# Optimization experiments

Hardware: AMD Instinct MI355X
Metric: run time of the kernel (lower is better)

The kernel has to match this reference:

```python
import jax, jax.numpy as jnp
import numpy as np

N, E, B = 8192, 131072, 256
F_ATOM, D, H, HD, L, FC, BINS = 92, 256, 8, 32, 6, 512, 256
VMIN, VMAX = 0.0, 8.0


def layer_norm(x, g, b, eps=1e-5):
    mu = jnp.mean(x, axis=-1, keepdims=True)
    var = jnp.var(x, axis=-1, keepdims=True)
    return (x - mu) * jax.lax.rsqrt(var + eps) * g + b


def silu(x):
    return x * jax.nn.sigmoid(x)


def setup_inputs() -> dict:
    key = jax.random.key(0)
    ks = iter(jax.random.split(key, 80))

    def lin(fan_in, shape):
        return jax.random.normal(next(ks), shape, jnp.float32) / np.sqrt(fan_in)

    inp = {
        'x': jax.random.normal(next(ks), (N, F_ATOM), jnp.float32),
        'edge_attr': jax.random.normal(next(ks), (E, 3), jnp.float32) * 2.0,
        'edge_index': jax.random.randint(next(ks), (2, E), 0, N, dtype=jnp.int32),
        'batch': jnp.sort(jax.random.randint(next(ks), (N,), 0, B, dtype=jnp.int32)),
        # atom_embedding: Linear(92,256) -> LN -> SiLU -> Linear(256,256)
        'aw1': lin(F_ATOM, (F_ATOM, D)), 'ab1': jnp.zeros((D,)),
        'ag1': jnp.ones((D,)), 'abt1': jnp.zeros((D,)),
        'aw2': lin(D, (D, D)), 'ab2': jnp.zeros((D,)),
        # rbf MLP: Linear(256,256) LN SiLU Linear LN SiLU Linear
        'rw1': lin(BINS, (BINS, D)), 'rb1': jnp.zeros((D,)),
        'rg1': jnp.ones((D,)), 'rbt1': jnp.zeros((D,)),
        'rw2': lin(D, (D, D)), 'rb2': jnp.zeros((D,)),
        'rg2': jnp.ones((D,)), 'rbt2': jnp.zeros((D,)),
        'rw3': lin(D, (D, D)), 'rb3': jnp.zeros((D,)),
        # L stacked PrdnetConv (edge-conditioned multi-head graph attention)
        'Wq': lin(D, (L, D, D)), 'bq': jnp.zeros((L, D)),
        'Wk': lin(D, (L, D, D)), 'bk': jnp.zeros((L, D)),
        'Wv': lin(D, (L, D, D)), 'bv': jnp.zeros((L, D)),
        'We': lin(D, (L, D, D)), 'be': jnp.zeros((L, D)),
        'Wo': lin(D, (L, D, D)), 'bo': jnp.zeros((L, D)),
        'lng': jnp.ones((L, D)), 'lnb': jnp.zeros((L, D)),
        # FC head: Linear(256,512) then fc_out Linear(512,1)
        'fw1': lin(D, (D, FC)), 'fb1': jnp.zeros((FC,)),
        'fow': lin(FC, (FC, 1)), 'fob': jnp.zeros((1,)),
    }
    return inp


def _forward(x, edge_attr, edge_index, batch, aw1, ab1, ag1, abt1, aw2, ab2,
             rw1, rb1, rg1, rbt1, rw2, rb2, rg2, rbt2, rw3, rb3,
             Wq, bq, Wk, bk, Wv, bv, We, be, Wo, bo, lng, lnb,
             fw1, fb1, fow, fob):
    # atom embedding (dropout = identity at inference)
    node = silu(layer_norm(x @ aw1 + ab1, ag1, abt1)) @ aw2 + ab2  # [N, D]

    # RBF expansion of edge lengths, then edge MLP
    d = jnp.linalg.norm(edge_attr, axis=1)  # [E]
    centers = jnp.linspace(VMIN, VMAX, BINS)
    gamma = 1.0 / (centers[1] - centers[0]) ** 2
    rbf = jnp.exp(-gamma * (d[:, None] - centers[None, :]) ** 2)  # [E, BINS]
    e = silu(layer_norm(rbf @ rw1 + rb1, rg1, rbt1))
    e = silu(layer_norm(e @ rw2 + rb2, rg2, rbt2))
    e = e @ rw3 + rb3  # [E, D]

    src, dst = edge_index[0], edge_index[1]
    inv_sqrt = 1.0 / np.sqrt(HD)
    for l in range(L):
        res = node
        q = (node @ Wq[l] + bq[l]).reshape(N, H, HD)
        k = (node @ Wk[l] + bk[l]).reshape(N, H, HD)
        v = (node @ Wv[l] + bv[l]).reshape(N, H, HD)
        ee = (e @ We[l] + be[l]).reshape(E, H, HD)
        kj = k[src] + ee  # edge-conditioned keys [E, H, HD]
        vj = v[src] + ee  # edge-conditioned values
        score = jnp.sum(q[dst] * kj, axis=-1) * inv_sqrt  # [E, H]
        smax = jax.ops.segment_max(score, dst, num_segments=N)  # [N, H]
        ex = jnp.exp(score - smax[dst])
        den = jax.ops.segment_sum(ex, dst, num_segments=N)
        alpha = ex / (den[dst] + 1e-16)  # neighborhood softmax [E, H]
        msg = jax.ops.segment_sum(alpha[:, :, None] * vj, dst, num_segments=N)
        out = msg.reshape(N, D) @ Wo[l] + bo[l]
        out = layer_norm(out, lng[l], lnb[l])
        node = out + res  # residual

    # scatter-mean graph pooling
    sums = jax.ops.segment_sum(node, batch, num_segments=B)  # [B, D]
    cnt = jax.ops.segment_sum(jnp.ones((N,), node.dtype), batch, num_segments=B)
    feats = sums / jnp.clip(cnt, 1.0)[:, None]

    feats = feats @ fw1 + fb1  # single fc layer: no act (i == len-1 in source)
    return feats @ fow + fob  # [B, 1], identity link


def reference(x, edge_attr, edge_index, batch, aw1, ab1, ag1, abt1, aw2, ab2,
              rw1, rb1, rg1, rbt1, rw2, rb2, rg2, rbt2, rw3, rb3,
              Wq, bq, Wk, bk, Wv, bv, We, be, Wo, bo, lng, lnb,
              fw1, fb1, fow, fob):
    return _forward(x, edge_attr, edge_index, batch, aw1, ab1, ag1, abt1, aw2,
                    ab2, rw1, rb1, rg1, rbt1, rw2, rb2, rg2, rbt2, rw3, rb3,
                    Wq, bq, Wk, bk, Wv, bv, We, be, Wo, bo, lng, lnb,
                    fw1, fb1, fow, fob)
```

## Files before the change

kernel.cpp:

```cpp
#include <hip/hip_runtime.h>
#include <hip/hip_bf16.h>
#include <cstddef>

#define NN    8192
#define EE    131072
#define BB    256
#define F_AT  92
#define DD    256
#define HH    8
#define HDIM  32
#define LL    6
#define FCD   512

typedef __hip_bfloat16 bf16;
typedef __attribute__((ext_vector_type(8))) __bf16 bf16x8;
typedef __attribute__((ext_vector_type(4))) float f32x4;

__device__ __forceinline__ float to_f(float x) { return x; }
__device__ __forceinline__ float to_f(bf16 x) { return __bfloat162float(x); }
__device__ __forceinline__ float bfu(unsigned short u) {
    return __uint_as_float(((unsigned)u) << 16);
}
__device__ __forceinline__ unsigned short bfbits(float x) {
    bf16 h = __float2bfloat16(x);
    return *(unsigned short*)&h;
}
__device__ __forceinline__ void store_v(float* p, float v) { *p = v; }
__device__ __forceinline__ void store_v(bf16* p, float v) { *p = __float2bfloat16(v); }

__device__ __forceinline__ float4 load4(const float* p) { return *(const float4*)p; }
__device__ __forceinline__ float4 load4(const bf16* p) {
    const ushort4 r = *(const ushort4*)p;
    return make_float4(bfu(r.x), bfu(r.y), bfu(r.z), bfu(r.w));
}

__device__ __forceinline__ void store_f4(float* p, const float4& f) {
    *(float4*)p = f;
}
__device__ __forceinline__ void store_f4(bf16* p, const float4& f) {
    ushort4 u = {bfbits(f.x), bfbits(f.y), bfbits(f.z), bfbits(f.w)};
    *(ushort4*)p = u;
}

__device__ __forceinline__ bf16x8 ld8(const bf16* p) { return *(const bf16x8*)p; }
__device__ __forceinline__ bf16x8 ld8(const float* p) {
    const float4 f0 = *(const float4*)p;
    const float4 f1 = *(const float4*)(p + 4);
    bf16x8 r;
    r[0] = (__bf16)f0.x; r[1] = (__bf16)f0.y; r[2] = (__bf16)f0.z; r[3] = (__bf16)f0.w;
    r[4] = (__bf16)f1.x; r[5] = (__bf16)f1.y; r[6] = (__bf16)f1.z; r[7] = (__bf16)f1.w;
    return r;
}

__device__ __forceinline__ void async_copy16(const void* g, void* l) {
    __builtin_amdgcn_global_load_lds(
        (const __attribute__((address_space(1))) unsigned int*)g,
        (__attribute__((address_space(3))) unsigned int*)l, 16, 0, 0);
}

__global__ __launch_bounds__(256) void transpose_weights(
    const float* __restrict__ rw1, const float* __restrict__ rw2,
    const float* __restrict__ rw3, const float* __restrict__ aw2,
    const float* __restrict__ Wq, const float* __restrict__ Wk,
    const float* __restrict__ Wv, const float* __restrict__ We,
    const float* __restrict__ Wo, __bf16* __restrict__ out)
{
    __shared__ float tile[64][65];
    const int midx = blockIdx.y;
    const float* src;
    if (midx == 0) src = rw1;
    else if (midx == 1) src = rw2;
    else if (midx == 2) src = rw3;
    else if (midx == 3) src = aw2;
    else {
        const int l = (midx - 4) / 5, s = (midx - 4) % 5;
        const float* bases[5] = {Wq, Wk, Wv, We, Wo};
        src = bases[s] + (size_t)l * 65536;
    }
    __bf16* dst = out + (size_t)midx * 65536;
    const int k0 = (blockIdx.x >> 2) * 64;
    const int n0 = (blockIdx.x & 3) * 64;
    const int c = threadIdx.x & 63;
    const int r0 = threadIdx.x >> 6;
#pragma unroll
    for (int p = 0; p < 16; ++p) {
        const int r = r0 + p * 4;
        tile[r][c] = src[(size_t)(k0 + r) * 256 + n0 + c];
    }
    __syncthreads();
#pragma unroll
    for (int p = 0; p < 16; ++p) {
        const int n = r0 + p * 4;
        dst[(size_t)(n0 + n) * 256 + k0 + c] = (__bf16)tile[c][n];
    }
}

__global__ __launch_bounds__(256) void pack_qkv_bias(
    const float* __restrict__ bq, const float* __restrict__ bk,
    const float* __restrict__ bv, float* __restrict__ out)
{
    const int i = blockIdx.x * 256 + threadIdx.x;
    if (i >= LL * 768) return;
    const int l = i / 768, r = i % 768;
    const float* s = (r < 256) ? bq : (r < 512) ? bk : bv;
    out[i] = s[l * 256 + (r & 255)];
}

__global__ __launch_bounds__(256) void combine_w3e(
    const float* __restrict__ rw3, const float* __restrict__ We,
    __bf16* __restrict__ Wt_out)
{
    __shared__ float As[16][65];
    __shared__ float Ws[16][65];
    const int l = blockIdx.z;
    const float* W = We + (size_t)l * 65536;
    __bf16* dst = Wt_out + (size_t)l * 65536;
    const int m0 = blockIdx.x * 64;
    const int n0 = blockIdx.y * 64;
    const int tid = threadIdx.x;
    const int tx = tid & 15, ty = tid >> 4;
    float acc[4][4] = {};

    for (int k0 = 0; k0 < 256; k0 += 16) {
        {
            const int ar = tid >> 2;
            const int ac = (tid & 3) * 4;
#pragma unroll
            for (int j = 0; j < 4; ++j)
                As[ac + j][ar] = rw3[(size_t)(m0 + ar) * 256 + k0 + ac + j];
        }
        {
            const int wr = tid >> 4;
            const int wc = (tid & 15) * 4;
#pragma unroll
            for (int j = 0; j < 4; ++j)
                Ws[wr][wc + j] = W[(size_t)(k0 + wr) * 256 + n0 + wc + j];
        }
        __syncthreads();
#pragma unroll
        for (int kk = 0; kk < 16; ++kk) {
            float a[4], b[4];
#pragma unroll
            for (int i = 0; i < 4; ++i) a[i] = As[kk][ty * 4 + i];
#pragma unroll
            for (int j = 0; j < 4; ++j) b[j] = Ws[kk][tx * 4 + j];
#pragma unroll
            for (int i = 0; i < 4; ++i)
#pragma unroll
                for (int j = 0; j < 4; ++j) acc[i][j] += a[i] * b[j];
        }
        __syncthreads();
    }
#pragma unroll
    for (int i = 0; i < 4; ++i) {
        const int gk = m0 + ty * 4 + i;
#pragma unroll
        for (int j = 0; j < 4; ++j) {
            const int gn = n0 + tx * 4 + j;
            dst[(size_t)gn * 256 + gk] = (__bf16)acc[i][j];
        }
    }
}

__global__ __launch_bounds__(256) void combine_bias(
    const float* __restrict__ rb3, const float* __restrict__ We,
    const float* __restrict__ be, float* __restrict__ out)
{
    const int l = blockIdx.x;
    const int n = threadIdx.x;
    const float* W = We + (size_t)l * 65536;
    float s = be[l * 256 + n];
    for (int m = 0; m < 256; ++m) s += rb3[m] * W[m * 256 + n];
    out[l * 256 + n] = s;
}

__global__ __launch_bounds__(256) void mfma_gemm_ln(
    const bf16* __restrict__ A, const __bf16* __restrict__ Wt,
    const float* __restrict__ bias, const float* __restrict__ g,
    const float* __restrict__ b, bf16* __restrict__ C, int do_silu)
{
    __shared__ __align__(16) __bf16 As[64 * 64];
    __shared__ __align__(16) __bf16 Bs[256 * 64];
    const int tid = threadIdx.x;
    const int m0 = blockIdx.x * 64;
    const int wave = tid >> 6, lane = tid & 63;
    const int lm = lane & 15, lq = lane >> 4;
    const int lrow = lane >> 3;
    const int lcolsw = ((lane & 7) ^ lrow) * 8;

    f32x4 acc[16] = {};

    for (int k0 = 0; k0 < 256; k0 += 64) {
#pragma unroll
        for (int p = 0; p < 2; ++p) {
            const int rbase = wave * 16 + p * 8;
            async_copy16(A + (size_t)(m0 + rbase + lrow) * 256 + k0 + lcolsw,
                         As + rbase * 64);
        }
#pragma unroll
        for (int p = 0; p < 8; ++p) {
            const int rbase = wave * 64 + p * 8;
            async_copy16(Wt + (size_t)(rbase + lrow) * 256 + k0 + lcolsw,
                         Bs + rbase * 64);
        }
        __syncthreads();
#pragma unroll
        for (int ks = 0; ks < 2; ++ks) {
            const int sw = ((ks * 4 + lq) ^ (lm & 7)) * 8;
            const bf16x8 a = *(const bf16x8*)(As + (wave * 16 + lm) * 64 + sw);
#pragma unroll
            for (int j = 0; j < 16; ++j) {
                const bf16x8 bf = *(const bf16x8*)(Bs + (j * 16 + lm) * 64 + sw);
                acc[j] = __builtin_amdgcn_mfma_f32_16x16x32_bf16(a, bf, acc[j], 0, 0, 0);
            }
        }
        __syncthreads();
    }

    float gg[16], bb[16];
#pragma unroll
    for (int j = 0; j < 16; ++j) {
        const float bv = bias[j * 16 + lm];
        gg[j] = g[j * 16 + lm];
        bb[j] = b[j * 16 + lm];
#pragma unroll
        for (int r = 0; r < 4; ++r) acc[j][r] += bv;
    }

#pragma unroll
    for (int r = 0; r < 4; ++r) {
        float s = 0.f, q = 0.f;
#pragma unroll
        for (int j = 0; j < 16; ++j) { const float v = acc[j][r]; s += v; q += v * v; }
#pragma unroll
        for (int msk = 1; msk < 16; msk <<= 1) {
            s += __shfl_xor(s, msk);
            q += __shfl_xor(q, msk);
        }
        const float mean = s * (1.f / 256.f);
        const float var = q * (1.f / 256.f) - mean * mean;
        const float rs = rsqrtf(var + 1e-5f);
        bf16* crow = C + (size_t)(m0 + wave * 16 + lq * 4 + r) * 256;
#pragma unroll
        for (int j = 0; j < 16; ++j) {
            float v = (acc[j][r] - mean) * rs * gg[j] + bb[j];
            if (do_silu) v = v / (1.f + __expf(-v));
            crow[j * 16 + lm] = __float2bfloat16(v);
        }
    }
}

template <typename CT>
__global__ __launch_bounds__(256) void mfma_gemm_async(
    const bf16* __restrict__ A, const __bf16* __restrict__ Wt,
    const float* __restrict__ bias, CT* __restrict__ C,
    int M, int Nn, int K)
{
    __shared__ __align__(16) __bf16 As[128 * 64];
    __shared__ __align__(16) __bf16 Bs[128 * 64];
    const int tid = threadIdx.x;
    const int m0 = blockIdx.y * 128;
    const int n0 = blockIdx.x * 128;
    const int wave = tid >> 6, lane = tid & 63;
    const int wm = (wave & 1) * 64, wn = (wave >> 1) * 64;
    const int lm = lane & 15, lq = lane >> 4;
    const int lrow = lane >> 3;
    const int lcolsw = ((lane & 7) ^ lrow) * 8;

    f32x4 acc[4][4] = {};

    for (int k0 = 0; k0 < K; k0 += 64) {
#pragma unroll
        for (int p = 0; p < 4; ++p) {
            const int rbase = wave * 32 + p * 8;
            async_copy16(A  + (size_t)(m0 + rbase + lrow) * K + k0 + lcolsw,
                         As + rbase * 64);
            async_copy16(Wt + (size_t)(n0 + rbase + lrow) * K + k0 + lcolsw,
                         Bs + rbase * 64);
        }
        __syncthreads();
#pragma unroll
        for (int ks = 0; ks < 2; ++ks) {
            const int sw = ((ks * 4 + lq) ^ (lm & 7)) * 8;
            bf16x8 a[4], b[4];
#pragma unroll
            for (int i = 0; i < 4; ++i) {
                a[i] = *(const bf16x8*)(As + (wm + i * 16 + lm) * 64 + sw);
                b[i] = *(const bf16x8*)(Bs + (wn + i * 16 + lm) * 64 + sw);
            }
#pragma unroll
            for (int i = 0; i < 4; ++i)
#pragma unroll
                for (int j = 0; j < 4; ++j)
                    acc[i][j] = __builtin_amdgcn_mfma_f32_16x16x32_bf16(
                        a[i], b[j], acc[i][j], 0, 0, 0);
        }
        __syncthreads();
    }

#pragma unroll
    for (int i = 0; i < 4; ++i) {
        const int gm = m0 + wm + i * 16 + lq * 4;
#pragma unroll
        for (int j = 0; j < 4; ++j) {
            const int gn = n0 + wn + j * 16 + lm;
            const float bv = bias ? bias[gn] : 0.f;
#pragma unroll
            for (int r = 0; r < 4; ++r)
                store_v(&C[(size_t)(gm + r) * Nn + gn], acc[i][j][r] + bv);
        }
    }
}

template <typename AT, typename CT>
__global__ __launch_bounds__(256) void mfma_gemm(
    const AT* __restrict__ A, const __bf16* __restrict__ Wt,
    const float* __restrict__ bias, CT* __restrict__ C,
    int M, int Nn, int K)
{
    __shared__ __align__(16) __bf16 As[128 * 72];
    __shared__ __align__(16) __bf16 Bs[128 * 72];
    const int tid = threadIdx.x;
    const int m0 = blockIdx.x * 128;
    const int n0 = blockIdx.y * 128;
    const int wave = tid >> 6, lane = tid & 63;
    const int wm = (wave & 1) * 64, wn = (wave >> 1) * 64;
    const int lm = lane & 15, lq = lane >> 4;

    f32x4 acc[4][4] = {};

    const int srow = tid >> 3;
    const int scol = (tid & 7) * 8;

    for (int k0 = 0; k0 < K; k0 += 64) {
#pragma unroll
        for (int p = 0; p < 4; ++p) {
            const int r = srow + 32 * p;
            *(bf16x8*)(As + r * 72 + scol) = ld8(A + (size_t)(m0 + r) * K + k0 + scol);
            *(bf16x8*)(Bs + r * 72 + scol) = *(const bf16x8*)(Wt + (size_t)(n0 + r) * K + k0 + scol);
        }
        __syncthreads();
#pragma unroll
        for (int ks = 0; ks < 2; ++ks) {
            bf16x8 a[4], b[4];
#pragma unroll
            for (int i = 0; i < 4; ++i) {
                a[i] = *(const bf16x8*)(As + (wm + i * 16 + lm) * 72 + ks * 32 + lq * 8);
                b[i] = *(const bf16x8*)(Bs + (wn + i * 16 + lm) * 72 + ks * 32 + lq * 8);
            }
#pragma unroll
            for (int i = 0; i < 4; ++i)
#pragma unroll
                for (int j = 0; j < 4; ++j)
                    acc[i][j] = __builtin_amdgcn_mfma_f32_16x16x32_bf16(
                        a[i], b[j], acc[i][j], 0, 0, 0);
        }
        __syncthreads();
    }

#pragma unroll
    for (int i = 0; i < 4; ++i) {
        const int gm = m0 + wm + i * 16 + lq * 4;
#pragma unroll
        for (int j = 0; j < 4; ++j) {
            const int gn = n0 + wn + j * 16 + lm;
            const float bv = bias ? bias[gn] : 0.f;
#pragma unroll
            for (int r = 0; r < 4; ++r)
                store_v(&C[(size_t)(gm + r) * Nn + gn], acc[i][j][r] + bv);
        }
    }
}

template <typename AT, typename CT>
__global__ __launch_bounds__(256) void gemm_bias(
    const AT* __restrict__ A, const float* __restrict__ W,
    const float* __restrict__ bias, CT* __restrict__ C,
    int M, int Nn, int K)
{
    __shared__ float As[16][65];
    __shared__ float Ws[16][65];
    const int m0 = blockIdx.x * 64;
    const int n0 = blockIdx.y * 64;
    const int tid = threadIdx.x;
    const int tx = tid & 15, ty = tid >> 4;
    float acc[4][4] = {};

    for (int k0 = 0; k0 < K; k0 += 16) {
        {
            const int ar = tid >> 2;
            const int ac = (tid & 3) * 4;
            const int gm = m0 + ar;
#pragma unroll
            for (int j = 0; j < 4; ++j) {
                const int gk = k0 + ac + j;
                float v = 0.f;
                if (gm < M && gk < K) v = to_f(A[(size_t)gm * K + gk]);
                As[ac + j][ar] = v;
            }
        }
        {
            const int wr = tid >> 4;
            const int wc = (tid & 15) * 4;
            const int gk = k0 + wr;
#pragma unroll
            for (int j = 0; j < 4; ++j) {
                float v = 0.f;
                if (gk < K) v = W[(size_t)gk * Nn + n0 + wc + j];
                Ws[wr][wc + j] = v;
            }
        }
        __syncthreads();
#pragma unroll
        for (int kk = 0; kk < 16; ++kk) {
            float a[4], b[4];
#pragma unroll
            for (int i = 0; i < 4; ++i) a[i] = As[kk][ty * 4 + i];
#pragma unroll
            for (int j = 0; j < 4; ++j) b[j] = Ws[kk][tx * 4 + j];
#pragma unroll
            for (int i = 0; i < 4; ++i)
#pragma unroll
                for (int j = 0; j < 4; ++j) acc[i][j] += a[i] * b[j];
        }
        __syncthreads();
    }
#pragma unroll
    for (int i = 0; i < 4; ++i) {
        const int gm = m0 + ty * 4 + i;
        if (gm >= M) continue;
#pragma unroll
        for (int j = 0; j < 4; ++j) {
            const int gn = n0 + tx * 4 + j;
            float v = acc[i][j];
            if (bias) v += bias[gn];
            store_v(&C[(size_t)gm * Nn + gn], v);
        }
    }
}

__global__ __launch_bounds__(256) void rbf_kernel(
    const float* __restrict__ ea, const int* __restrict__ eid,
    bf16* __restrict__ rbf)
{
    const int p = blockIdx.x * 4 + (threadIdx.x >> 6);
    const int e = eid[p];
    const int c0 = (threadIdx.x & 63) * 4;
    const float ax = ea[e * 3 + 0];
    const float ay = ea[e * 3 + 1];
    const float az = ea[e * 3 + 2];
    const float d = sqrtf(ax * ax + ay * ay + az * az);
    const float step = 8.0f / 255.0f;
    const float gamma = 1.0f / (step * step);
    float o[4];
#pragma unroll
    for (int j = 0; j < 4; ++j) {
        const float t = d - (float)(c0 + j) * step;
        o[j] = __expf(-gamma * t * t);
    }
    store_f4(rbf + (size_t)p * DD + c0, make_float4(o[0], o[1], o[2], o[3]));
}

template <typename XT, typename YT>
__global__ __launch_bounds__(256) void ln_act_kernel(
    const XT* __restrict__ X, YT* __restrict__ Y,
    const float* __restrict__ g, const float* __restrict__ b,
    const float* __restrict__ resid, int rows, int do_silu)
{
    const int wave = threadIdx.x >> 6;
    const int lane = threadIdx.x & 63;
    const int r = blockIdx.x * 4 + wave;
    if (r >= rows) return;
    const float4 x = load4(X + (size_t)r * DD + lane * 4);
    float s = x.x + x.y + x.z + x.w;
    float q = x.x * x.x + x.y * x.y + x.z * x.z + x.w * x.w;
    for (int off = 32; off; off >>= 1) {
        s += __shfl_down(s, off);
        q += __shfl_down(q, off);
    }
    s = __shfl(s, 0);
    q = __shfl(q, 0);
    const float mean = s * (1.f / 256.f);
    const float var = q * (1.f / 256.f) - mean * mean;
    const float rs = rsqrtf(var + 1e-5f);
    const int c = lane * 4;
    float xs[4] = {x.x, x.y, x.z, x.w};
    float out[4];
#pragma unroll
    for (int i = 0; i < 4; ++i) {
        float v = (xs[i] - mean) * rs * g[c + i] + b[c + i];
        if (do_silu) v = v / (1.f + __expf(-v));
        out[i] = v;
    }
    if (resid) {
        const float4 rv = load4(resid + (size_t)r * DD + c);
        out[0] += rv.x; out[1] += rv.y; out[2] += rv.z; out[3] += rv.w;
    }
    store_f4(Y + (size_t)r * DD + c, make_float4(out[0], out[1], out[2], out[3]));
}

__global__ __launch_bounds__(256) void deg_kernel(
    const int* __restrict__ dst, int* __restrict__ deg)
{
    const int e = blockIdx.x * 256 + threadIdx.x;
    if (e < EE) atomicAdd(&deg[dst[e]], 1);
}

__global__ __launch_bounds__(256) void csr_scan(
    const int* __restrict__ deg, int* __restrict__ rowptr)
{
    __shared__ int part[256];
    const int t = threadIdx.x;
    int local[32];
    int s = 0;
#pragma unroll
    for (int i = 0; i < 32; ++i) { local[i] = deg[t * 32 + i]; s += local[i]; }
    part[t] = s;
    __syncthreads();
    if (t == 0) {
        int run = 0;
        for (int i = 0; i < 256; ++i) { const int v = part[i]; part[i] = run; run += v; }
    }
    __syncthreads();
    int run = part[t];
#pragma unroll
    for (int i = 0; i < 32; ++i) { rowptr[t * 32 + i] = run; run += local[i]; }
    if (t == 255) rowptr[NN] = run;
}

__global__ __launch_bounds__(256) void fill_kernel(
    const int* __restrict__ src, const int* __restrict__ dst,
    const int* __restrict__ rowptr, int* __restrict__ fill,
    int* __restrict__ eid, int* __restrict__ srcc)
{
    const int e = blockIdx.x * 256 + threadIdx.x;
    if (e >= EE) return;
    const int d = dst[e];
    const int pos = atomicAdd(&fill[d], 1);
    const int q = rowptr[d] + pos;
    eid[q] = e;
    srcc[q] = src[e];
}

__global__ __launch_bounds__(256) void attn_kernel(
    const bf16* __restrict__ qkv, const bf16* __restrict__ ee, int estride,
    const int* __restrict__ rowptr, const int* __restrict__ srcc,
    float* __restrict__ msg)
{
    const int n = blockIdx.x;
    const int tid = threadIdx.x;
    const int wave = tid >> 6, lane = tid & 63;
    const int e0 = rowptr[n];
    const int deg = rowptr[n + 1] - e0;

    if (deg == 0) {
        msg[(size_t)n * DD + tid] = 0.f;
        return;
    }

    __shared__ float wm[4][HH];
    __shared__ float wl[4][HH];
    __shared__ float wacc[4][DD];

    const float4 qreg = load4(qkv + (size_t)n * 768 + lane * 4);

    float m = -3.402823466e38f, l = 0.f;
    float4 acc = {0.f, 0.f, 0.f, 0.f};

    int j = wave;
    float4 kv = {0.f, 0.f, 0.f, 0.f};
    float4 vv = kv, ev = kv;
    if (j < deg) {
        const int e = e0 + j;
        const bf16* srow = qkv + (size_t)srcc[e] * 768;
        kv = load4(srow + 256 + lane * 4);
        vv = load4(srow + 512 + lane * 4);
        ev = load4(ee + (size_t)e * estride + lane * 4);
    }
    while (j < deg) {
        const int jn = j + 4;
        float4 kv2 = {0.f, 0.f, 0.f, 0.f};
        float4 vv2 = kv2, ev2 = kv2;
        if (jn < deg) {
            const int e2 = e0 + jn;
            const bf16* srow2 = qkv + (size_t)srcc[e2] * 768;
            kv2 = load4(srow2 + 256 + lane * 4);
            vv2 = load4(srow2 + 512 + lane * 4);
            ev2 = load4(ee + (size_t)e2 * estride + lane * 4);
        }
        float p = qreg.x * (kv.x + ev.x) + qreg.y * (kv.y + ev.y) +
                  qreg.z * (kv.z + ev.z) + qreg.w * (kv.w + ev.w);
        p += __shfl_down(p, 4);
        p += __shfl_down(p, 2);
        p += __shfl_down(p, 1);
        const float s = __shfl(p, lane & 56) * 0.17677669529663687f;
        const float mnew = fmaxf(m, s);
        const float scale = __expf(m - mnew);
        const float pe = __expf(s - mnew);
        l = l * scale + pe;
        acc.x = acc.x * scale + pe * (vv.x + ev.x);
        acc.y = acc.y * scale + pe * (vv.y + ev.y);
        acc.z = acc.z * scale + pe * (vv.z + ev.z);
        acc.w = acc.w * scale + pe * (vv.w + ev.w);
        m = mnew;
        kv = kv2; vv = vv2; ev = ev2;
        j = jn;
    }

    if ((lane & 7) == 0) { wm[wave][lane >> 3] = m; wl[wave][lane >> 3] = l; }
    *(float4*)(&wacc[wave][lane * 4]) = acc;
    __syncthreads();

    {
        const int c = tid, h = tid >> 5;
        float M = wm[0][h];
#pragma unroll
        for (int i = 1; i < 4; ++i) M = fmaxf(M, wm[i][h]);
        float L = 0.f, num = 0.f;
#pragma unroll
        for (int i = 0; i < 4; ++i) {
            const float sc = __expf(wm[i][h] - M);
            L += wl[i][h] * sc;
            num += wacc[i][c] * sc;
        }
        msg[(size_t)n * DD + c] = num / (L + 1e-16f);
    }
}

__global__ __launch_bounds__(256) void zero_kernel(float* __restrict__ p, int n)
{
    const int i = blockIdx.x * 256 + threadIdx.x;
    if (i < n) p[i] = 0.f;
}

__global__ __launch_bounds__(256) void pool_kernel(
    const float* __restrict__ node, const int* __restrict__ batch,
    float* __restrict__ sums, float* __restrict__ cnt)
{
    const int n = blockIdx.x;
    const int c = threadIdx.x;
    const int b = batch[n];
    atomicAdd(&sums[b * DD + c], node[(size_t)n * DD + c]);
    if (c == 0) atomicAdd(&cnt[b], 1.0f);
}

__global__ __launch_bounds__(256) void pooled_kernel(
    const float* __restrict__ sums, const float* __restrict__ cnt,
    float* __restrict__ pooled)
{
    const int b = blockIdx.x;
    const int c = threadIdx.x;
    float cc = cnt[b];
    if (cc < 1.f) cc = 1.f;
    pooled[b * DD + c] = sums[b * DD + c] / cc;
}

__global__ __launch_bounds__(64) void final_kernel(
    const float* __restrict__ fc, const float* __restrict__ fow,
    const float* __restrict__ fob, float* __restrict__ out)
{
    const int b = blockIdx.x;
    const int lane = threadIdx.x;
    float s = 0.f;
#pragma unroll
    for (int i = lane; i < FCD; i += 64) s += fc[(size_t)b * FCD + i] * fow[i];
    for (int off = 32; off; off >>= 1) s += __shfl_down(s, off);
    if (lane == 0) out[b] = s + fob[0];
}

extern "C" void kernel_launch(void* const* d_in, const int* in_sizes, int n_in,
                              void* d_out, int out_size, void* d_ws,
                              size_t ws_size, hipStream_t stream)
{
    const float* x         = (const float*)d_in[0];
    const float* edge_attr = (const float*)d_in[1];
    const int*   eidx      = (const int*)d_in[2];
    const int*   batch     = (const int*)d_in[3];
    const float* aw1 = (const float*)d_in[4];
    const float* ab1 = (const float*)d_in[5];
    const float* ag1 = (const float*)d_in[6];
    const float* abt1 = (const float*)d_in[7];
    const float* aw2 = (const float*)d_in[8];
    const float* ab2 = (const float*)d_in[9];
    const float* rw1 = (const float*)d_in[10];
    const float* rb1 = (const float*)d_in[11];
    const float* rg1 = (const float*)d_in[12];
    const float* rbt1 = (const float*)d_in[13];
    const float* rw2 = (const float*)d_in[14];
    const float* rb2 = (const float*)d_in[15];
    const float* rg2 = (const float*)d_in[16];
    const float* rbt2 = (const float*)d_in[17];
    const float* rw3 = (const float*)d_in[18];
    const float* rb3 = (const float*)d_in[19];
    const float* Wq = (const float*)d_in[20];
    const float* bq = (const float*)d_in[21];
    const float* Wk = (const float*)d_in[22];
    const float* bk = (const float*)d_in[23];
    const float* Wv = (const float*)d_in[24];
    const float* bv = (const float*)d_in[25];
    const float* We_ = (const float*)d_in[26];
    const float* be_ = (const float*)d_in[27];
    const float* Wo = (const float*)d_in[28];
    const float* bo = (const float*)d_in[29];
    const float* lng = (const float*)d_in[30];
    const float* lnb = (const float*)d_in[31];
    const float* fw1 = (const float*)d_in[32];
    const float* fb1 = (const float*)d_in[33];
    const float* fow = (const float*)d_in[34];
    const float* fob = (const float*)d_in[35];

    const int* src = eidx;
    const int* dst = eidx + EE;

    char* w = (char*)d_ws;
    size_t off = 0;
    auto alloc = [&](size_t bytes) -> void* {
        void* p = w + off;
        off += (bytes + 255) & ~(size_t)255;
        return p;
    };
    bf16* t_buf = (bf16*)alloc((size_t)EE * DD * 2);
    float* node = (float*)alloc((size_t)NN * DD * 4);
    bf16*  qkv  = (bf16*)alloc((size_t)NN * 768 * 2);
    float* msg  = (float*)alloc((size_t)NN * DD * 4);
    float* outb = (float*)alloc((size_t)NN * DD * 4);
    int* deg    = (int*)alloc((size_t)NN * 4);
    int* fillc  = (int*)alloc((size_t)NN * 4);
    int* rowptr = (int*)alloc((size_t)(NN + 1) * 4);
    int* eid    = (int*)alloc((size_t)EE * 4);
    int* srcc   = (int*)alloc((size_t)EE * 4);
    float* sums  = (float*)alloc((size_t)BB * DD * 4);
    float* cnt   = (float*)alloc((size_t)BB * 4);
    float* pooled = (float*)alloc((size_t)BB * DD * 4);
    float* fc    = (float*)alloc((size_t)BB * FCD * 4);
    __bf16* Wt  = (__bf16*)alloc((size_t)40 * 65536 * 2);
    float* qkvb = (float*)alloc((size_t)LL * 768 * 4);
    float* be_c = (float*)alloc((size_t)LL * 256 * 4);

    const size_t avail = (off <= ws_size) ? ws_size - off : 0;
    int G = 1;
    if      (avail >= (size_t)EE * (6 * DD) * 2 + 256) G = 6;
    else if (avail >= (size_t)EE * (3 * DD) * 2 + 256) G = 3;
    else if (avail >= (size_t)EE * (2 * DD) * 2 + 256) G = 2;
    bf16* e_slab = (bf16*)alloc((size_t)EE * (G * DD) * 2);
    (void)n_in; (void)in_sizes; (void)out_size;

    const dim3 blk(256);
    auto WT = [&](int i) -> const __bf16* { return Wt + (size_t)i * 65536; };

    hipLaunchKernelGGL(transpose_weights, dim3(16, 34), blk, 0, stream,
                       rw1, rw2, rw3, aw2, Wq, Wk, Wv, We_, Wo, Wt);
    hipLaunchKernelGGL(combine_w3e, dim3(4, 4, LL), blk, 0, stream, rw3, We_, Wt + (size_t)34 * 65536);
    hipLaunchKernelGGL(combine_bias, dim3(LL), blk, 0, stream, rb3, We_, be_, be_c);
    hipLaunchKernelGGL(pack_qkv_bias, dim3((LL * 768 + 255) / 256), blk, 0, stream, bq, bk, bv, qkvb);
    hipLaunchKernelGGL(zero_kernel, dim3((2 * NN + 255) / 256), blk, 0, stream, (float*)deg, 2 * NN);
    hipLaunchKernelGGL(deg_kernel, dim3(EE / 256), blk, 0, stream, dst, deg);
    hipLaunchKernelGGL(csr_scan, dim3(1), blk, 0, stream, deg, rowptr);
    hipLaunchKernelGGL(fill_kernel, dim3(EE / 256), blk, 0, stream, src, dst, rowptr, fillc, eid, srcc);

    hipLaunchKernelGGL(rbf_kernel, dim3(EE / 4), blk, 0, stream, edge_attr, eid, t_buf);
    hipLaunchKernelGGL(mfma_gemm_ln, dim3(EE / 64), blk, 0, stream, t_buf, WT(0), rb1, rg1, rbt1, e_slab, 1);
    hipLaunchKernelGGL(mfma_gemm_ln, dim3(EE / 64), blk, 0, stream, e_slab, WT(1), rb2, rg2, rbt2, t_buf, 1);

    {
        dim3 gn64(NN / 64, DD / 64);
        hipLaunchKernelGGL((gemm_bias<float, float>), gn64, blk, 0, stream, x, aw1, ab1, outb, NN, DD, F_AT);
        hipLaunchKernelGGL((ln_act_kernel<float, float>), dim3(NN / 4), blk, 0, stream, outb, outb, ag1, abt1, (const float*)nullptr, NN, 1);
        hipLaunchKernelGGL((mfma_gemm<float, float>), dim3(NN / 128, DD / 128), blk, 0, stream, outb, WT(3), ab2, node, NN, DD, DD);
    }

    for (int l = 0; l < LL; ++l) {
        const size_t bo_ = (size_t)l * DD;
        hipLaunchKernelGGL((mfma_gemm<float, bf16>), dim3(NN / 128, 768 / 128), blk, 0, stream,
                           node, WT(4 + 5 * l), qkvb + (size_t)l * 768, qkv, NN, 768, DD);
        if (l % G == 0) {
            hipLaunchKernelGGL((mfma_gemm_async<bf16>), dim3((G * DD) / 128, EE / 128), blk, 0, stream,
                               t_buf, WT(34 + l), be_c + (size_t)l * 256, e_slab, EE, G * DD, DD);
        }
        const bf16* ee_l = e_slab + (size_t)(l % G) * DD;
        hipLaunchKernelGGL(attn_kernel, dim3(NN), blk, 0, stream, qkv, ee_l, G * DD, rowptr, srcc, msg);
        hipLaunchKernelGGL((mfma_gemm<float, float>), dim3(NN / 128, DD / 128), blk, 0, stream, msg, WT(8 + 5 * l), bo + bo_, outb, NN, DD, DD);
        hipLaunchKernelGGL((ln_act_kernel<float, float>), dim3(NN / 4), blk, 0, stream, outb, node, lng + bo_, lnb + bo_, node, NN, 0);
    }

    const int PZ = BB * DD + BB;
    hipLaunchKernelGGL(zero_kernel, dim3((PZ + 255) / 256), blk, 0, stream, sums, PZ);
    hipLaunchKernelGGL(pool_kernel, dim3(NN), blk, 0, stream, node, batch, sums, cnt);
    hipLaunchKernelGGL(pooled_kernel, dim3(BB), blk, 0, stream, sums, cnt, pooled);
    {
        dim3 gf(BB / 64, FCD / 64);
        hipLaunchKernelGGL((gemm_bias<float, float>), gf, blk, 0, stream, pooled, fw1, fb1, fc, BB, FCD, DD);
    }
    hipLaunchKernelGGL(final_kernel, dim3(BB), dim3(64), 0, stream, fc, fow, fob, (float*)d_out);
}
```

Measured before the change: 1.001 ms.

## Stage GEMM epilogues through LDS for coalesced stores and remap tiles per XCD

The LN-fused edge GEMM now writes its normalized bf16 tile into shared memory and then copies it to global memory as coalesced 16-byte vectors, replacing scattered 2-byte stores. The edge-feature GEMM (renamed mfma_gemm_ee) gets the same LDS-staged epilogue and a 1D grid remapped so each group of blocks sharing blockIdx.x mod 8 handles a contiguous range of M rows, aiming to improve L2 locality per XCD. The cost is an extra barrier and shared-memory round trip, and the remap assumes the M tile count divides evenly by 8.

```diff
diff --git a/kernel.cpp b/kernel.cpp
--- a/kernel.cpp
+++ b/kernel.cpp
@@ -240,27 +240,42 @@
         const float mean = s * (1.f / 256.f);
         const float var = q * (1.f / 256.f) - mean * mean;
         const float rs = rsqrtf(var + 1e-5f);
-        bf16* crow = C + (size_t)(m0 + wave * 16 + lq * 4 + r) * 256;
+        __bf16* erow = Bs + (wave * 16 + lq * 4 + r) * 256;
 #pragma unroll
         for (int j = 0; j < 16; ++j) {
             float v = (acc[j][r] - mean) * rs * gg[j] + bb[j];
             if (do_silu) v = v / (1.f + __expf(-v));
-            crow[j * 16 + lm] = __float2bfloat16(v);
-        }
-    }
-}
-
-template <typename CT>
-__global__ __launch_bounds__(256) void mfma_gemm_async(
+            erow[j * 16 + lm] = (__bf16)v;
+        }
+    }
+    __syncthreads();
+    {
+        __bf16* cbase = (__bf16*)C + (size_t)m0 * 256;
+#pragma unroll
+        for (int p = 0; p < 8; ++p) {
+            const int ofs = (tid + p * 256) * 8;
+            *(bf16x8*)(cbase + ofs) = *(const bf16x8*)(Bs + ofs);
+        }
+    }
+}
+
+__global__ __launch_bounds__(256) void mfma_gemm_ee(
     const bf16* __restrict__ A, const __bf16* __restrict__ Wt,
-    const float* __restrict__ bias, CT* __restrict__ C,
+    const float* __restrict__ bias, bf16* __restrict__ C,
     int M, int Nn, int K)
 {
-    __shared__ __align__(16) __bf16 As[128 * 64];
-    __shared__ __align__(16) __bf16 Bs[128 * 64];
+    __shared__ __align__(16) __bf16 smem[128 * 128];
+    __bf16* As = smem;
+    __bf16* Bs = smem + 128 * 64;
     const int tid = threadIdx.x;
-    const int m0 = blockIdx.y * 128;
-    const int n0 = blockIdx.x * 128;
+
+    const int nt_n = Nn >> 7;
+    const int xcd = blockIdx.x & 7;
+    const int local = blockIdx.x >> 3;
+    const int per_xcd = (M >> 7) >> 3;
+    const int m0 = (xcd * per_xcd + local / nt_n) * 128;
+    const int n0 = (local % nt_n) * 128;
+
     const int wave = tid >> 6, lane = tid & 63;
     const int wm = (wave & 1) * 64, wn = (wave >> 1) * 64;
     const int lm = lane & 15, lq = lane >> 4;
@@ -300,15 +315,24 @@
 
 #pragma unroll
     for (int i = 0; i < 4; ++i) {
-        const int gm = m0 + wm + i * 16 + lq * 4;
+        const int rl = wm + i * 16 + lq * 4;
 #pragma unroll
         for (int j = 0; j < 4; ++j) {
-            const int gn = n0 + wn + j * 16 + lm;
-            const float bv = bias ? bias[gn] : 0.f;
+            const int cl = wn + j * 16 + lm;
+            const float bb = bias ? bias[n0 + cl] : 0.f;
 #pragma unroll
             for (int r = 0; r < 4; ++r)
-                store_v(&C[(size_t)(gm + r) * Nn + gn], acc[i][j][r] + bv);
-        }
+                smem[(rl + r) * 128 + cl] = (__bf16)(acc[i][j][r] + bb);
+        }
+    }
+    __syncthreads();
+#pragma unroll
+    for (int p = 0; p < 8; ++p) {
+        const int ch = tid + p * 256;
+        const int row = ch >> 4;
+        const int col = (ch & 15) * 8;
+        *(bf16x8*)((__bf16*)C + (size_t)(m0 + row) * Nn + n0 + col) =
+            *(const bf16x8*)(smem + row * 128 + col);
     }
 }
 
@@ -774,7 +798,8 @@
         hipLaunchKernelGGL((mfma_gemm<float, bf16>), dim3(NN / 128, 768 / 128), blk, 0, stream,
                            node, WT(4 + 5 * l), qkvb + (size_t)l * 768, qkv, NN, 768, DD);
         if (l % G == 0) {
-            hipLaunchKernelGGL((mfma_gemm_async<bf16>), dim3((G * DD) / 128, EE / 128), blk, 0, stream,
+            const int nblocks = (EE / 128) * ((G * DD) / 128);
+            hipLaunchKernelGGL(mfma_gemm_ee, dim3(nblocks), blk, 0, stream,
                                t_buf, WT(34 + l), be_c + (size_t)l * 256, e_slab, EE, G * DD, DD);
         }
         const bf16* ee_l = e_slab + (size_t)(l % G) * DD;
```

Measured after the change: 966.8 us. 1.03x faster.
